# Kernel optimization log

Hardware: AMD Instinct MI355X
Metric: run time of the kernel (lower is better)

Reference implementation:

```python
import jax, jax.numpy as jnp
import numpy as np


def setup_inputs() -> dict:
    N, E, D, C = 100000, 100000, 512, 512
    key = jax.random.key(0)
    k = jax.random.split(key, 6)
    x = jax.random.normal(k[0], (N, D), dtype=jnp.float32)
    W = jax.random.normal(k[1], (D, 3 * C), dtype=jnp.float32) * (1.0 / np.sqrt(D))
    bias = jax.random.normal(k[2], (C,), dtype=jnp.float32) * (1.0 / np.sqrt(C))
    eta = jax.random.uniform(k[3], (E, 3, 1), dtype=jnp.float32)
    src = jax.random.randint(k[4], (E,), 0, N, dtype=jnp.int32)
    dst = jax.random.randint(k[5], (E,), 0, N, dtype=jnp.int32)
    return {"x": x, "W": W, "bias": bias, "eta": eta, "src": src, "dst": dst}


def reference(x, W, bias, eta, src, dst):
    N = x.shape[0]
    C = bias.shape[0]
    # projection: [N, D] @ [D, 3C] -> [N, 3, C]
    h = jnp.matmul(x, W).reshape(N, 3, C)
    # message: src node state scaled by per-edge eta [E,3,1]
    msg = h[src] * eta  # [E, 3, C]
    # reduce: sum messages into destination nodes (nodes w/o in-edges -> 0)
    agg = jax.ops.segment_sum(msg, dst, num_segments=N)  # [N, 3, C]
    # sum over the 3 positional slots, add bias, tanh
    return jnp.tanh(agg.sum(axis=1) + bias)
```

## Files before the change

### kernel.cpp

```cpp
#include <hip/hip_runtime.h>

typedef _Float16 half_t;
typedef __attribute__((ext_vector_type(8))) _Float16 half8;
typedef __attribute__((ext_vector_type(4))) float floatx4;

#define BM 128
#define BN 128
#define BK 32

__global__ void cvt_w_kernel(const float* __restrict__ W, half_t* __restrict__ Wt,
                             int D, int C, int total) {
    int idx = blockIdx.x * blockDim.x + threadIdx.x;
    if (idx >= total) return;
    int c = idx / 1536;
    int r = idx - c * 1536;
    int s = r >> 9;
    int d = r & 511;
    Wt[idx] = (half_t)W[(long)d * 1536 + s * 512 + c];
}

__global__ void tanh_bias_kernel(const float* __restrict__ bias, float* __restrict__ tb, int C) {
    int c = blockIdx.x * blockDim.x + threadIdx.x;
    if (c >= C) return;
    float ex = __expf(2.0f * bias[c]);
    tb[c] = 1.0f - 2.0f / (ex + 1.0f);
}

__global__ void hist_kernel(const int* __restrict__ dst, int* __restrict__ deg, int E) {
    int e = blockIdx.x * blockDim.x + threadIdx.x;
    if (e < E) atomicAdd(&deg[dst[e]], 1);
}

__global__ void scan_partial2_kernel(const int* __restrict__ deg,
                                     int* __restrict__ bsum, int* __restrict__ bsum2, int n) {
    __shared__ int wsum[4], wsum2[4];
    int t = threadIdx.x, lane = t & 63, w = t >> 6;
    int base = blockIdx.x * 1024 + t * 4;
    int s = 0, s2 = 0;
#pragma unroll
    for (int j = 0; j < 4; ++j) {
        int i = base + j;
        if (i < n) { int d = deg[i]; s += d; s2 += (d > 0); }
    }
#pragma unroll
    for (int o = 1; o < 64; o <<= 1) { s += __shfl_xor(s, o); s2 += __shfl_xor(s2, o); }
    if (lane == 0) { wsum[w] = s; wsum2[w] = s2; }
    __syncthreads();
    if (t == 0) {
        bsum[blockIdx.x]  = wsum[0]  + wsum[1]  + wsum[2]  + wsum[3];
        bsum2[blockIdx.x] = wsum2[0] + wsum2[1] + wsum2[2] + wsum2[3];
    }
}

__device__ int exscan_wave128(int* arr, int nb, int lane) {
    int a0 = (lane < nb) ? arr[lane] : 0;
    int a1 = (64 + lane < nb) ? arr[64 + lane] : 0;
    int s0 = a0, s1 = a1;
#pragma unroll
    for (int o = 1; o < 64; o <<= 1) {
        int t0 = __shfl_up(s0, o); if (lane >= o) s0 += t0;
        int t1 = __shfl_up(s1, o); if (lane >= o) s1 += t1;
    }
    s1 += __shfl(s0, 63);
    int tot = __shfl(s1, 63);
    if (lane < nb) arr[lane] = s0 - a0;
    if (64 + lane < nb) arr[64 + lane] = s1 - a1;
    return tot;
}

__global__ void scan_bsums2_kernel(int* __restrict__ bsum, int* __restrict__ bsum2,
                                   int nb, int* __restrict__ mc) {
    int lane = threadIdx.x & 63;
    if (nb <= 128) {
        exscan_wave128(bsum, nb, lane);
        int tot = exscan_wave128(bsum2, nb, lane);
        if (lane == 0) *mc = tot;
    } else if (lane == 0) {
        int acc = 0, acc2 = 0;
        for (int i = 0; i < nb; ++i) {
            int v = bsum[i];  bsum[i] = acc;   acc += v;
            int v2 = bsum2[i]; bsum2[i] = acc2; acc2 += v2;
        }
        *mc = acc2;
    }
}

__global__ void scan_final2_kernel(const int* __restrict__ deg,
                                   const int* __restrict__ bsum, const int* __restrict__ bsum2,
                                   int* __restrict__ off, int* __restrict__ rank,
                                   int* __restrict__ nodeid, int n) {
    __shared__ int wsum[4], wsum2[4];
    int t = threadIdx.x, lane = t & 63, w = t >> 6;
    int base = blockIdx.x * 1024 + t * 4;
    int v[4]; int s = 0, s2 = 0;
#pragma unroll
    for (int j = 0; j < 4; ++j) {
        int i = base + j;
        v[j] = (i < n) ? deg[i] : 0;
        s += v[j]; s2 += (v[j] > 0);
    }
    int sc = s, sc2 = s2;
#pragma unroll
    for (int o = 1; o < 64; o <<= 1) {
        int u  = __shfl_up(sc, o);  if (lane >= o) sc  += u;
        int u2 = __shfl_up(sc2, o); if (lane >= o) sc2 += u2;
    }
    if (lane == 63) { wsum[w] = sc; wsum2[w] = sc2; }
    __syncthreads();
    int woff = 0, woff2 = 0;
    for (int i = 0; i < w; ++i) { woff += wsum[i]; woff2 += wsum2[i]; }
    int ex  = bsum[blockIdx.x]  + woff  + (sc  - s);
    int ex2 = bsum2[blockIdx.x] + woff2 + (sc2 - s2);
#pragma unroll
    for (int j = 0; j < 4; ++j) {
        int i = base + j;
        if (i < n) {
            off[i] = ex;
            if (v[j] > 0) { rank[i] = ex2; nodeid[ex2] = i; ex2++; }
            ex += v[j];
        }
    }
}

__global__ void scatter_kernel(const int* __restrict__ dst, const int* __restrict__ off,
                               int* __restrict__ cursor, int* __restrict__ eidx, int E) {
    int e = blockIdx.x * blockDim.x + threadIdx.x;
    if (e >= E) return;
    int d = dst[e];
    int p = off[d] + atomicAdd(&cursor[d], 1);
    eidx[p] = e;
}

__global__ __launch_bounds__(256) void aggx_kernel(
    const float* __restrict__ x, const float* __restrict__ eta,
    const int* __restrict__ src, const int* __restrict__ off,
    const int* __restrict__ deg, const int* __restrict__ rank,
    const int* __restrict__ eidx, half_t* __restrict__ Z, int N, int D)
{
    int node = blockIdx.x * 4 + (threadIdx.x >> 6);
    if (node >= N) return;
    int d = deg[node];
    if (d == 0) return;
    int lane = threadIdx.x & 63;

    float a0[8] = {}, a1[8] = {}, a2[8] = {};
    int start = off[node];
    for (int q = 0; q < d; ++q) {
        int e = eidx[start + q];
        int s = src[e];
        float e0 = eta[3 * e + 0], e1 = eta[3 * e + 1], e2 = eta[3 * e + 2];
        const float* xr = x + (long)s * D + lane * 8;
        floatx4 v0 = *(const floatx4*)xr;
        floatx4 v1 = *(const floatx4*)(xr + 4);
#pragma unroll
        for (int j = 0; j < 4; ++j) {
            a0[j] += e0 * v0[j]; a0[j + 4] += e0 * v1[j];
            a1[j] += e1 * v0[j]; a1[j + 4] += e1 * v1[j];
            a2[j] += e2 * v0[j]; a2[j + 4] += e2 * v1[j];
        }
    }
    half_t* zr = Z + (long)rank[node] * (3 * D) + lane * 8;
    half8 h0, h1, h2;
#pragma unroll
    for (int j = 0; j < 8; ++j) { h0[j] = (half_t)a0[j]; h1[j] = (half_t)a1[j]; h2[j] = (half_t)a2[j]; }
    *(half8*)zr = h0;
    *(half8*)(zr + D) = h1;
    *(half8*)(zr + 2 * D) = h2;
}

__global__ __launch_bounds__(256) void fill_kernel(const int* __restrict__ deg,
                                                   const float* __restrict__ tb,
                                                   float* __restrict__ out, int N, int C) {
    int node = blockIdx.x * 4 + (threadIdx.x >> 6);
    if (node >= N || deg[node] != 0) return;
    int lane = threadIdx.x & 63;
    float* o = out + (long)node * C;
    for (int c0 = lane * 8; c0 < C; c0 += 64 * 8) {
        floatx4 v0 = *(const floatx4*)(tb + c0);
        floatx4 v1 = *(const floatx4*)(tb + c0 + 4);
        *(floatx4*)(o + c0) = v0;
        *(floatx4*)(o + c0 + 4) = v1;
    }
}

__global__ __launch_bounds__(256) void gemm_tanh_kernel(
    const half_t* __restrict__ A,
    const half_t* __restrict__ Bt,
    const float* __restrict__ bias,
    const int* __restrict__ mc_ptr,
    const int* __restrict__ nodeid,
    float* __restrict__ out,
    int K, int C)
{
    __shared__ half_t As[BM * BK];
    __shared__ half_t Bs[BN * BK];

    const int Mc = *mc_ptr;
    const int ncol = C / BN;
    const int T = ((Mc + BM - 1) / BM) * ncol;
    const int b = blockIdx.x;
    if (b >= T) return;
    const int qq = T >> 3, rem = T & 7;
    const int xcd = b & 7, ib = b >> 3;
    const int wg = (xcd < rem ? xcd * (qq + 1) : rem * (qq + 1) + (xcd - rem) * qq) + ib;
    const int n0 = (wg % ncol) * BN;
    const int m0 = (wg / ncol) * BM;

    const int t    = threadIdx.x;
    const int lane = t & 63;
    const int wave = t >> 6;
    const int wm   = (wave >> 1) * 64;
    const int wn   = (wave & 1) * 64;

    const int r1 = t >> 2;
    const int r2 = r1 + 64;
    const int k8 = (((t & 3) ^ ((t >> 3) & 3))) * 8;
    const long gA1 = (long)(m0 + r1) * K + k8;
    const long gA2 = (long)(m0 + r2) * K + k8;
    const long gB1 = (long)(n0 + r1) * K + k8;
    const long gB2 = (long)(n0 + r2) * K + k8;

    floatx4 acc[4][4] = {};

    const int mrow = wm + (lane & 15);
    const int nrow = wn + (lane & 15);
    const int koff = (((lane >> 4) ^ ((lane >> 1) & 3))) * 8;

    for (int kt = 0; kt < K; kt += BK) {
        __builtin_amdgcn_global_load_lds(
            (const __attribute__((address_space(1))) void*)(A + gA1 + kt),
            (__attribute__((address_space(3))) void*)(As + t * 8), 16, 0, 0);
        __builtin_amdgcn_global_load_lds(
            (const __attribute__((address_space(1))) void*)(A + gA2 + kt),
            (__attribute__((address_space(3))) void*)(As + (t + 256) * 8), 16, 0, 0);
        __builtin_amdgcn_global_load_lds(
            (const __attribute__((address_space(1))) void*)(Bt + gB1 + kt),
            (__attribute__((address_space(3))) void*)(Bs + t * 8), 16, 0, 0);
        __builtin_amdgcn_global_load_lds(
            (const __attribute__((address_space(1))) void*)(Bt + gB2 + kt),
            (__attribute__((address_space(3))) void*)(Bs + (t + 256) * 8), 16, 0, 0);
        __syncthreads();

        half8 af[4], bf[4];
#pragma unroll
        for (int i = 0; i < 4; ++i)
            af[i] = *(const half8*)&As[(mrow + i * 16) * BK + koff];
#pragma unroll
        for (int i = 0; i < 4; ++i)
            bf[i] = *(const half8*)&Bs[(nrow + i * 16) * BK + koff];
#pragma unroll
        for (int i = 0; i < 4; ++i)
#pragma unroll
            for (int j = 0; j < 4; ++j)
                acc[i][j] = __builtin_amdgcn_mfma_f32_16x16x32_f16(af[i], bf[j], acc[i][j], 0, 0, 0);
        __syncthreads();
    }

    const int col0 = lane & 15;
    const int rbase = (lane >> 4) * 4;
    float bj[4];
#pragma unroll
    for (int j = 0; j < 4; ++j)
        bj[j] = bias[n0 + wn + col0 + j * 16];
#pragma unroll
    for (int i = 0; i < 4; ++i) {
#pragma unroll
        for (int rr = 0; rr < 4; ++rr) {
            int crow = m0 + wm + i * 16 + rbase + rr;
            if (crow >= Mc) continue;
            long base = (long)nodeid[crow] * C + n0 + wn + col0;
#pragma unroll
            for (int j = 0; j < 4; ++j) {
                float xv = acc[i][j][rr] + bj[j];
                float ex = __expf(2.0f * xv);
                out[base + j * 16] = 1.0f - 2.0f / (ex + 1.0f);
            }
        }
    }
}

extern "C" void kernel_launch(void* const* d_in, const int* in_sizes, int n_in,
                              void* d_out, int out_size, void* d_ws, size_t ws_size,
                              hipStream_t stream) {
    const float* x    = (const float*)d_in[0];
    const float* W    = (const float*)d_in[1];
    const float* bias = (const float*)d_in[2];
    const float* eta  = (const float*)d_in[3];
    const int*   src  = (const int*)d_in[4];
    const int*   dst  = (const int*)d_in[5];
    float* out = (float*)d_out;

    const int  C   = in_sizes[2];
    const int  C3  = 3 * C;
    const int  D   = in_sizes[1] / C3;
    const long xcount = in_sizes[0];
    const int  N   = (int)(xcount / D);
    const int  E   = in_sizes[4];
    const int  K   = 3 * D;
    const int  Npad = ((N + BM - 1) / BM) * BM;
    const int  nb  = (N + 1023) / 1024;
    const size_t nbPad = (size_t)((nb + 3) & ~3);

    char* ws = (char*)d_ws;
    size_t o = 0;
    half_t* Z    = (half_t*)(ws + o); o += (size_t)Npad * K * sizeof(half_t);
    half_t* Wt_h = (half_t*)(ws + o); o += (size_t)C * K * sizeof(half_t);
    int* deg     = (int*)(ws + o);    o += (size_t)N * sizeof(int);
    int* cursor  = (int*)(ws + o);    o += (size_t)N * sizeof(int);
    int* off     = (int*)(ws + o);    o += (size_t)N * sizeof(int);
    int* rank    = (int*)(ws + o);    o += (size_t)N * sizeof(int);
    int* nodeid  = (int*)(ws + o);    o += (size_t)N * sizeof(int);
    int* eidx    = (int*)(ws + o);    o += (size_t)E * sizeof(int);
    int* bsum    = (int*)(ws + o);    o += nbPad * sizeof(int);
    int* bsum2   = (int*)(ws + o);    o += nbPad * sizeof(int);
    int* mc      = (int*)(ws + o);    o += 4 * sizeof(int);
    float* tb    = (float*)(ws + o);  o += (size_t)C * sizeof(float);

    hipMemsetAsync(deg, 0, 2 * (size_t)N * sizeof(int), stream);
    cvt_w_kernel<<<(C * K + 255) / 256, 256, 0, stream>>>(W, Wt_h, D, C, C * K);
    tanh_bias_kernel<<<(C + 255) / 256, 256, 0, stream>>>(bias, tb, C);
    hist_kernel<<<(E + 255) / 256, 256, 0, stream>>>(dst, deg, E);
    scan_partial2_kernel<<<nb, 256, 0, stream>>>(deg, bsum, bsum2, N);
    scan_bsums2_kernel<<<1, 64, 0, stream>>>(bsum, bsum2, nb, mc);
    scan_final2_kernel<<<nb, 256, 0, stream>>>(deg, bsum, bsum2, off, rank, nodeid, N);
    scatter_kernel<<<(E + 255) / 256, 256, 0, stream>>>(dst, off, cursor, eidx, E);
    aggx_kernel<<<(N + 3) / 4, 256, 0, stream>>>(x, eta, src, off, deg, rank, eidx, Z, N, D);
    fill_kernel<<<(N + 3) / 4, 256, 0, stream>>>(deg, tb, out, N, C);
    {
        const int nwg = ((N + BM - 1) / BM) * (C / BN);
        gemm_tanh_kernel<<<nwg, 256, 0, stream>>>(Z, Wt_h, bias, mc, nodeid, out, K, C);
    }
}
```

Baseline: 579.3 us.

## Double-buffer GEMM LDS, presort edge data in scatter, fuse small kernels

The GEMM main loop now uses two LDS buffers: the next K tile is issued with global_load_lds while the current one is multiplied, which cuts the number of barriers that expose load latency. The scatter kernel now writes src ids and padded eta vectors in CSR order, so the aggregation loop reads them contiguously instead of through an eidx indirection. The bias-tanh kernel is folded into the weight-conversion kernel, and the zero-degree fill is folded into the aggregation kernel, which removes two launches. The cost is double the GEMM LDS footprint (which may lower occupancy) and extra workspace and write traffic for the 16-byte eta records.

```diff
diff --git a/kernel.cpp b/kernel.cpp
--- a/kernel.cpp
+++ b/kernel.cpp
@@ -9,21 +9,19 @@
 #define BK 32
 
 __global__ void cvt_w_kernel(const float* __restrict__ W, half_t* __restrict__ Wt,
+                             const float* __restrict__ bias, float* __restrict__ tb,
                              int D, int C, int total) {
     int idx = blockIdx.x * blockDim.x + threadIdx.x;
     if (idx >= total) return;
+    if (idx < C) {
+        float ex = __expf(2.0f * bias[idx]);
+        tb[idx] = 1.0f - 2.0f / (ex + 1.0f);
+    }
     int c = idx / 1536;
     int r = idx - c * 1536;
     int s = r >> 9;
     int d = r & 511;
     Wt[idx] = (half_t)W[(long)d * 1536 + s * 512 + c];
-}
-
-__global__ void tanh_bias_kernel(const float* __restrict__ bias, float* __restrict__ tb, int C) {
-    int c = blockIdx.x * blockDim.x + threadIdx.x;
-    if (c >= C) return;
-    float ex = __expf(2.0f * bias[c]);
-    tb[c] = 1.0f - 2.0f / (ex + 1.0f);
 }
 
 __global__ void hist_kernel(const int* __restrict__ dst, int* __restrict__ deg, int E) {
@@ -122,41 +120,55 @@
     }
 }
 
-__global__ void scatter_kernel(const int* __restrict__ dst, const int* __restrict__ off,
-                               int* __restrict__ cursor, int* __restrict__ eidx, int E) {
+__global__ void scatter_kernel(const int* __restrict__ dst, const int* __restrict__ src,
+                               const float* __restrict__ eta,
+                               const int* __restrict__ off, int* __restrict__ cursor,
+                               int* __restrict__ srcs, floatx4* __restrict__ etas, int E) {
     int e = blockIdx.x * blockDim.x + threadIdx.x;
     if (e >= E) return;
     int d = dst[e];
     int p = off[d] + atomicAdd(&cursor[d], 1);
-    eidx[p] = e;
+    srcs[p] = src[e];
+    floatx4 et;
+    et[0] = eta[3 * e + 0]; et[1] = eta[3 * e + 1]; et[2] = eta[3 * e + 2]; et[3] = 0.0f;
+    etas[p] = et;
 }
 
 __global__ __launch_bounds__(256) void aggx_kernel(
-    const float* __restrict__ x, const float* __restrict__ eta,
-    const int* __restrict__ src, const int* __restrict__ off,
+    const float* __restrict__ x, const int* __restrict__ srcs,
+    const floatx4* __restrict__ etas, const int* __restrict__ off,
     const int* __restrict__ deg, const int* __restrict__ rank,
-    const int* __restrict__ eidx, half_t* __restrict__ Z, int N, int D)
+    const float* __restrict__ tb, float* __restrict__ out,
+    half_t* __restrict__ Z, int N, int D, int C)
 {
     int node = blockIdx.x * 4 + (threadIdx.x >> 6);
     if (node >= N) return;
+    int lane = threadIdx.x & 63;
     int d = deg[node];
-    if (d == 0) return;
-    int lane = threadIdx.x & 63;
+    if (d == 0) {
+        float* o = out + (long)node * C;
+        for (int c0 = lane * 8; c0 < C; c0 += 64 * 8) {
+            floatx4 v0 = *(const floatx4*)(tb + c0);
+            floatx4 v1 = *(const floatx4*)(tb + c0 + 4);
+            *(floatx4*)(o + c0) = v0;
+            *(floatx4*)(o + c0 + 4) = v1;
+        }
+        return;
+    }
 
     float a0[8] = {}, a1[8] = {}, a2[8] = {};
     int start = off[node];
     for (int q = 0; q < d; ++q) {
-        int e = eidx[start + q];
-        int s = src[e];
-        float e0 = eta[3 * e + 0], e1 = eta[3 * e + 1], e2 = eta[3 * e + 2];
+        int s = srcs[start + q];
+        floatx4 et = etas[start + q];
         const float* xr = x + (long)s * D + lane * 8;
         floatx4 v0 = *(const floatx4*)xr;
         floatx4 v1 = *(const floatx4*)(xr + 4);
 #pragma unroll
         for (int j = 0; j < 4; ++j) {
-            a0[j] += e0 * v0[j]; a0[j + 4] += e0 * v1[j];
-            a1[j] += e1 * v0[j]; a1[j + 4] += e1 * v1[j];
-            a2[j] += e2 * v0[j]; a2[j + 4] += e2 * v1[j];
+            a0[j] += et[0] * v0[j]; a0[j + 4] += et[0] * v1[j];
+            a1[j] += et[1] * v0[j]; a1[j + 4] += et[1] * v1[j];
+            a2[j] += et[2] * v0[j]; a2[j + 4] += et[2] * v1[j];
         }
     }
     half_t* zr = Z + (long)rank[node] * (3 * D) + lane * 8;
@@ -166,21 +178,6 @@
     *(half8*)zr = h0;
     *(half8*)(zr + D) = h1;
     *(half8*)(zr + 2 * D) = h2;
-}
-
-__global__ __launch_bounds__(256) void fill_kernel(const int* __restrict__ deg,
-                                                   const float* __restrict__ tb,
-                                                   float* __restrict__ out, int N, int C) {
-    int node = blockIdx.x * 4 + (threadIdx.x >> 6);
-    if (node >= N || deg[node] != 0) return;
-    int lane = threadIdx.x & 63;
-    float* o = out + (long)node * C;
-    for (int c0 = lane * 8; c0 < C; c0 += 64 * 8) {
-        floatx4 v0 = *(const floatx4*)(tb + c0);
-        floatx4 v1 = *(const floatx4*)(tb + c0 + 4);
-        *(floatx4*)(o + c0) = v0;
-        *(floatx4*)(o + c0 + 4) = v1;
-    }
 }
 
 __global__ __launch_bounds__(256) void gemm_tanh_kernel(
@@ -192,8 +189,8 @@
     float* __restrict__ out,
     int K, int C)
 {
-    __shared__ half_t As[BM * BK];
-    __shared__ half_t Bs[BN * BK];
+    __shared__ half_t As[2][BM * BK];
+    __shared__ half_t Bs[2][BN * BK];
 
     const int Mc = *mc_ptr;
     const int ncol = C / BN;
@@ -226,35 +223,58 @@
     const int nrow = wn + (lane & 15);
     const int koff = (((lane >> 4) ^ ((lane >> 1) & 3))) * 8;
 
-    for (int kt = 0; kt < K; kt += BK) {
-        __builtin_amdgcn_global_load_lds(
-            (const __attribute__((address_space(1))) void*)(A + gA1 + kt),
-            (__attribute__((address_space(3))) void*)(As + t * 8), 16, 0, 0);
-        __builtin_amdgcn_global_load_lds(
-            (const __attribute__((address_space(1))) void*)(A + gA2 + kt),
-            (__attribute__((address_space(3))) void*)(As + (t + 256) * 8), 16, 0, 0);
-        __builtin_amdgcn_global_load_lds(
-            (const __attribute__((address_space(1))) void*)(Bt + gB1 + kt),
-            (__attribute__((address_space(3))) void*)(Bs + t * 8), 16, 0, 0);
-        __builtin_amdgcn_global_load_lds(
-            (const __attribute__((address_space(1))) void*)(Bt + gB2 + kt),
-            (__attribute__((address_space(3))) void*)(Bs + (t + 256) * 8), 16, 0, 0);
-        __syncthreads();
-
-        half8 af[4], bf[4];
-#pragma unroll
-        for (int i = 0; i < 4; ++i)
-            af[i] = *(const half8*)&As[(mrow + i * 16) * BK + koff];
-#pragma unroll
-        for (int i = 0; i < 4; ++i)
-            bf[i] = *(const half8*)&Bs[(nrow + i * 16) * BK + koff];
-#pragma unroll
-        for (int i = 0; i < 4; ++i)
-#pragma unroll
-            for (int j = 0; j < 4; ++j)
-                acc[i][j] = __builtin_amdgcn_mfma_f32_16x16x32_f16(af[i], bf[j], acc[i][j], 0, 0, 0);
-        __syncthreads();
-    }
+#define STAGE(buf, kt)                                                                     \
+    do {                                                                                   \
+        __builtin_amdgcn_global_load_lds(                                                  \
+            (const __attribute__((address_space(1))) void*)(A + gA1 + (kt)),               \
+            (__attribute__((address_space(3))) void*)(&As[buf][t * 8]), 16, 0, 0);         \
+        __builtin_amdgcn_global_load_lds(                                                  \
+            (const __attribute__((address_space(1))) void*)(A + gA2 + (kt)),               \
+            (__attribute__((address_space(3))) void*)(&As[buf][(t + 256) * 8]), 16, 0, 0); \
+        __builtin_amdgcn_global_load_lds(                                                  \
+            (const __attribute__((address_space(1))) void*)(Bt + gB1 + (kt)),              \
+            (__attribute__((address_space(3))) void*)(&Bs[buf][t * 8]), 16, 0, 0);         \
+        __builtin_amdgcn_global_load_lds(                                                  \
+            (const __attribute__((address_space(1))) void*)(Bt + gB2 + (kt)),              \
+            (__attribute__((address_space(3))) void*)(&Bs[buf][(t + 256) * 8]), 16, 0, 0); \
+    } while (0)
+
+#define COMPUTE(buf)                                                                       \
+    do {                                                                                   \
+        half8 af[4], bf[4];                                                                \
+        _Pragma("unroll") for (int i = 0; i < 4; ++i)                                      \
+            af[i] = *(const half8*)&As[buf][(mrow + i * 16) * BK + koff];                   \
+        _Pragma("unroll") for (int i = 0; i < 4; ++i)                                      \
+            bf[i] = *(const half8*)&Bs[buf][(nrow + i * 16) * BK + koff];                   \
+        _Pragma("unroll") for (int i = 0; i < 4; ++i)                                      \
+            _Pragma("unroll") for (int j = 0; j < 4; ++j)                                  \
+                acc[i][j] = __builtin_amdgcn_mfma_f32_16x16x32_f16(af[i], bf[j],           \
+                                                                   acc[i][j], 0, 0, 0);   \
+    } while (0)
+
+    const int nsteps = K / BK;
+    STAGE(0, 0);
+    int cur = 0;
+    for (int ks = 1; ks < nsteps; ++ks) {
+        STAGE(cur ^ 1, ks * BK);
+        asm volatile("s_waitcnt vmcnt(4)" ::: "memory");
+        __builtin_amdgcn_sched_barrier(0);
+        __builtin_amdgcn_s_barrier();
+        __builtin_amdgcn_sched_barrier(0);
+        COMPUTE(cur);
+        __builtin_amdgcn_sched_barrier(0);
+        __builtin_amdgcn_s_barrier();
+        __builtin_amdgcn_sched_barrier(0);
+        cur ^= 1;
+    }
+    asm volatile("s_waitcnt vmcnt(0)" ::: "memory");
+    __builtin_amdgcn_sched_barrier(0);
+    __builtin_amdgcn_s_barrier();
+    __builtin_amdgcn_sched_barrier(0);
+    COMPUTE(cur);
+
+#undef STAGE
+#undef COMPUTE
 
     const int col0 = lane & 15;
     const int rbase = (lane >> 4) * 4;
@@ -301,6 +321,8 @@
     const int  nb  = (N + 1023) / 1024;
     const size_t nbPad = (size_t)((nb + 3) & ~3);
 
+    auto alignup = [](size_t v) { return (v + 15) & ~(size_t)15; };
+
     char* ws = (char*)d_ws;
     size_t o = 0;
     half_t* Z    = (half_t*)(ws + o); o += (size_t)Npad * K * sizeof(half_t);
@@ -310,22 +332,22 @@
     int* off     = (int*)(ws + o);    o += (size_t)N * sizeof(int);
     int* rank    = (int*)(ws + o);    o += (size_t)N * sizeof(int);
     int* nodeid  = (int*)(ws + o);    o += (size_t)N * sizeof(int);
-    int* eidx    = (int*)(ws + o);    o += (size_t)E * sizeof(int);
+    int* srcs    = (int*)(ws + o);    o += (size_t)E * sizeof(int);
+    o = alignup(o);
+    floatx4* etas = (floatx4*)(ws + o); o += (size_t)E * sizeof(floatx4);
     int* bsum    = (int*)(ws + o);    o += nbPad * sizeof(int);
     int* bsum2   = (int*)(ws + o);    o += nbPad * sizeof(int);
     int* mc      = (int*)(ws + o);    o += 4 * sizeof(int);
     float* tb    = (float*)(ws + o);  o += (size_t)C * sizeof(float);
 
     hipMemsetAsync(deg, 0, 2 * (size_t)N * sizeof(int), stream);
-    cvt_w_kernel<<<(C * K + 255) / 256, 256, 0, stream>>>(W, Wt_h, D, C, C * K);
-    tanh_bias_kernel<<<(C + 255) / 256, 256, 0, stream>>>(bias, tb, C);
+    cvt_w_kernel<<<(C * K + 255) / 256, 256, 0, stream>>>(W, Wt_h, bias, tb, D, C, C * K);
     hist_kernel<<<(E + 255) / 256, 256, 0, stream>>>(dst, deg, E);
     scan_partial2_kernel<<<nb, 256, 0, stream>>>(deg, bsum, bsum2, N);
     scan_bsums2_kernel<<<1, 64, 0, stream>>>(bsum, bsum2, nb, mc);
     scan_final2_kernel<<<nb, 256, 0, stream>>>(deg, bsum, bsum2, off, rank, nodeid, N);
-    scatter_kernel<<<(E + 255) / 256, 256, 0, stream>>>(dst, off, cursor, eidx, E);
-    aggx_kernel<<<(N + 3) / 4, 256, 0, stream>>>(x, eta, src, off, deg, rank, eidx, Z, N, D);
-    fill_kernel<<<(N + 3) / 4, 256, 0, stream>>>(deg, tb, out, N, C);
+    scatter_kernel<<<(E + 255) / 256, 256, 0, stream>>>(dst, src, eta, off, cursor, srcs, etas, E);
+    aggx_kernel<<<(N + 3) / 4, 256, 0, stream>>>(x, srcs, etas, off, deg, rank, tb, out, Z, N, D, C);
     {
         const int nwg = ((N + BM - 1) / BM) * (C / BN);
         gemm_tanh_kernel<<<nwg, 256, 0, stream>>>(Z, Wt_h, bias, mc, nodeid, out, K, C);
```

Measured after the change: 546.0 us. 1.06x faster.
